# Performance work log

Hardware: AMD Instinct MI355X
Metric: run time of the kernel (lower is better)

The kernel has to match this reference:

```python
import jax, jax.numpy as jnp
import numpy as np

THRESHOLD = 0.95
SECONDARY = 0.5


def setup_inputs() -> dict:
    key = jax.random.key(0)
    quantum_states = jax.random.normal(key, (8, 2048, 64), dtype=jnp.float32)
    return {"quantum_states": quantum_states}


def reference(quantum_states):
    # quantum_states: (B, N, D)
    B, N, D = quantum_states.shape
    # pairwise fidelity: (states @ states^T)^2 -> (B, N, N)
    dots = jnp.einsum("bnd,bmd->bnm", quantum_states, quantum_states)
    fid = dots * dots
    # edge weights: 1.0 if fid >= threshold, else SECONDARY if fid >= secondary, else 0
    w = jnp.where(fid >= THRESHOLD, jnp.float32(1.0),
                  jnp.where(fid >= SECONDARY, jnp.float32(SECONDARY), jnp.float32(0.0)))
    # zero out diagonal (only i < j pairs form edges)
    eye = jnp.eye(N, dtype=bool)
    w = jnp.where(eye[None, :, :], jnp.float32(0.0), w)
    # Laplacian L = D - W
    deg = jnp.sum(w, axis=-1)  # (B, N)
    lap = -w
    idx = jnp.arange(N)
    lap = lap.at[:, idx, idx].set(deg)
    return lap
```

## Files before the change

kernel.cpp:

```cpp
#include <hip/hip_runtime.h>

typedef __attribute__((ext_vector_type(8))) __bf16 bf16x8;
typedef __attribute__((ext_vector_type(4))) __bf16 bf16x4;
typedef __attribute__((ext_vector_type(4))) float f32x4;

#define LDST 72

__global__ __launch_bounds__(256) void lap_strip_kernel(
    const float* __restrict__ X, float* __restrict__ out, int N)
{
    const int b      = blockIdx.y;
    const int strip0 = blockIdx.x * 32;
    const int tid  = threadIdx.x;
    const int lane = tid & 63;
    const int w    = tid >> 6;
    const int t    = lane & 15;
    const int g    = lane >> 4;

    __shared__ __align__(16) unsigned short As[2][128 * LDST];
    __shared__ __align__(16) unsigned short Bs[32 * LDST];
    __shared__ float deg_part[4][32];

    const float* Xb   = X   + (size_t)b * N * 64;
    float*       outb = out + (size_t)b * N * N;

    {
        const float4* src = reinterpret_cast<const float4*>(Xb + (size_t)strip0 * 64);
#pragma unroll
        for (int it = 0; it < 2; ++it) {
            int idx = tid + it * 256;
            int r = idx >> 4, q = idx & 15;
            float4 v = src[idx];
            bf16x4 h = {(__bf16)v.x, (__bf16)v.y, (__bf16)v.z, (__bf16)v.w};
            *reinterpret_cast<bf16x4*>(&Bs[r * LDST + q * 4]) = h;
        }
    }

    float4 pre[8];
    {
        const float4* src = reinterpret_cast<const float4*>(Xb);
#pragma unroll
        for (int it = 0; it < 8; ++it) pre[it] = src[tid + it * 256];
#pragma unroll
        for (int it = 0; it < 8; ++it) {
            int idx = tid + it * 256;
            int r = idx >> 4, q = idx & 15;
            float4 v = pre[it];
            bf16x4 h = {(__bf16)v.x, (__bf16)v.y, (__bf16)v.z, (__bf16)v.w};
            *reinterpret_cast<bf16x4*>(&As[0][r * LDST + q * 4]) = h;
        }
    }
    __syncthreads();

    bf16x8 bfrag[2][2];
#pragma unroll
    for (int ks = 0; ks < 2; ++ks)
#pragma unroll
        for (int fj = 0; fj < 2; ++fj)
            bfrag[ks][fj] = *reinterpret_cast<const bf16x8*>(
                &Bs[(16 * fj + t) * LDST + ks * 32 + g * 8]);

    float rs[2] = {0.f, 0.f};
    int cur = 0;
    const int nct = N >> 7;
    const int diag_ct = strip0 >> 7;

    for (int ct = 0; ct < nct; ++ct) {
        if (ct + 1 < nct) {
            const float4* src = reinterpret_cast<const float4*>(Xb + (size_t)(ct + 1) * 128 * 64);
#pragma unroll
            for (int it = 0; it < 8; ++it) pre[it] = src[tid + it * 256];
        }

        f32x4 acc[2][2] = {};
#pragma unroll
        for (int ks = 0; ks < 2; ++ks) {
            const int koff = ks * 32 + g * 8;
            bf16x8 a[2];
#pragma unroll
            for (int fi = 0; fi < 2; ++fi)
                a[fi] = *reinterpret_cast<const bf16x8*>(
                    &As[cur][(32 * w + 16 * fi + t) * LDST + koff]);
#pragma unroll
            for (int fi = 0; fi < 2; ++fi)
#pragma unroll
                for (int fj = 0; fj < 2; ++fj)
                    acc[fi][fj] = __builtin_amdgcn_mfma_f32_16x16x32_bf16(
                        a[fi], bfrag[ks][fj], acc[fi][fj], 0, 0, 0);
        }

        const bool has_diag = (ct == diag_ct);
#pragma unroll
        for (int fj = 0; fj < 2; ++fj) {
            const int orow = strip0 + 16 * fj + t;
#pragma unroll
            for (int fi = 0; fi < 2; ++fi) {
                const int ocol0 = ct * 128 + 32 * w + 16 * fi + 4 * g;
                float wv[4];
#pragma unroll
                for (int r = 0; r < 4; ++r) {
                    const float d = acc[fi][fj][r];
                    float wt = (fabsf(d) >= 0.97467943f) ? 1.0f
                             : ((fabsf(d) >= 0.70710678f) ? 0.5f : 0.0f);
                    if (has_diag && (ocol0 + r == orow)) wt = 0.0f;
                    rs[fj] += wt;
                    wv[r] = -wt;
                }
                f32x4 st = {wv[0], wv[1], wv[2], wv[3]};
                f32x4* dst = reinterpret_cast<f32x4*>(&outb[(size_t)orow * N + ocol0]);
                if (has_diag) *dst = st;
                else __builtin_nontemporal_store(st, dst);
            }
        }

        if (ct + 1 < nct) {
#pragma unroll
            for (int it = 0; it < 8; ++it) {
                int idx = tid + it * 256;
                int r = idx >> 4, q = idx & 15;
                float4 v = pre[it];
                bf16x4 h = {(__bf16)v.x, (__bf16)v.y, (__bf16)v.z, (__bf16)v.w};
                *reinterpret_cast<bf16x4*>(&As[cur ^ 1][r * LDST + q * 4]) = h;
            }
        }
        __syncthreads();
        cur ^= 1;
    }

    rs[0] += __shfl_xor(rs[0], 16, 64); rs[0] += __shfl_xor(rs[0], 32, 64);
    rs[1] += __shfl_xor(rs[1], 16, 64); rs[1] += __shfl_xor(rs[1], 32, 64);
    if (g == 0) { deg_part[w][t] = rs[0]; deg_part[w][16 + t] = rs[1]; }
    __syncthreads();
    if (tid < 32) {
        float d = deg_part[0][tid] + deg_part[1][tid] + deg_part[2][tid] + deg_part[3][tid];
        const int rr = strip0 + tid;
        outb[(size_t)rr * N + rr] = d;
    }
}

extern "C" void kernel_launch(void* const* d_in, const int* in_sizes, int n_in,
                              void* d_out, int out_size, void* d_ws, size_t ws_size,
                              hipStream_t stream) {
    const float* X = (const float*)d_in[0];
    float* out = (float*)d_out;

    const int B = 8;
    const int D = 64;
    const int N = in_sizes[0] / (B * D);

    dim3 grid(N / 32, B);
    lap_strip_kernel<<<grid, dim3(256), 0, stream>>>(X, out, N);
}
```

Before: 34.96 us.

## Use 512-thread blocks with one 16-column fragment per wave and custom barriers

Doubles the block to 8 waves, and each wave now computes a single 16-column fragment per 128-column tile instead of two, so per-thread register use and work per wave both shrink. Batch and strip are interleaved in a flat 1D grid so that neighbouring blocks come from different batches. __syncthreads is replaced with an LDS-only waitcnt plus s_barrier inside the loop, which keeps outstanding global stores and prefetch loads from stalling the barrier. In exchange there are more waves to synchronize per tile, and less MFMA work per wave to hide latency.

```diff
diff --git a/kernel.cpp b/kernel.cpp
--- a/kernel.cpp
+++ b/kernel.cpp
@@ -6,11 +6,23 @@
 
 #define LDST 72
 
-__global__ __launch_bounds__(256) void lap_strip_kernel(
+__device__ __forceinline__ void lds_barrier() {
+    asm volatile("s_waitcnt lgkmcnt(0)" ::: "memory");
+    __builtin_amdgcn_s_barrier();
+    __builtin_amdgcn_sched_barrier(0);
+}
+__device__ __forceinline__ void full_barrier() {
+    asm volatile("s_waitcnt vmcnt(0) lgkmcnt(0)" ::: "memory");
+    __builtin_amdgcn_s_barrier();
+    __builtin_amdgcn_sched_barrier(0);
+}
+
+__global__ __launch_bounds__(512) void lap_strip_kernel(
     const float* __restrict__ X, float* __restrict__ out, int N)
 {
-    const int b      = blockIdx.y;
-    const int strip0 = blockIdx.x * 32;
+    const int flat   = blockIdx.x;
+    const int b      = flat & 7;
+    const int strip0 = (flat >> 3) * 32;
     const int tid  = threadIdx.x;
     const int lane = tid & 63;
     const int w    = tid >> 6;
@@ -19,38 +31,34 @@
 
     __shared__ __align__(16) unsigned short As[2][128 * LDST];
     __shared__ __align__(16) unsigned short Bs[32 * LDST];
-    __shared__ float deg_part[4][32];
+    __shared__ float deg_part[8][32];
 
     const float* Xb   = X   + (size_t)b * N * 64;
     float*       outb = out + (size_t)b * N * N;
 
     {
         const float4* src = reinterpret_cast<const float4*>(Xb + (size_t)strip0 * 64);
-#pragma unroll
-        for (int it = 0; it < 2; ++it) {
-            int idx = tid + it * 256;
-            int r = idx >> 4, q = idx & 15;
-            float4 v = src[idx];
-            bf16x4 h = {(__bf16)v.x, (__bf16)v.y, (__bf16)v.z, (__bf16)v.w};
-            *reinterpret_cast<bf16x4*>(&Bs[r * LDST + q * 4]) = h;
-        }
+        int r = tid >> 4, q = tid & 15;
+        float4 v = src[tid];
+        bf16x4 h = {(__bf16)v.x, (__bf16)v.y, (__bf16)v.z, (__bf16)v.w};
+        *reinterpret_cast<bf16x4*>(&Bs[r * LDST + q * 4]) = h;
     }
 
-    float4 pre[8];
+    float4 pre[4];
     {
         const float4* src = reinterpret_cast<const float4*>(Xb);
 #pragma unroll
-        for (int it = 0; it < 8; ++it) pre[it] = src[tid + it * 256];
+        for (int it = 0; it < 4; ++it) pre[it] = src[tid + it * 512];
 #pragma unroll
-        for (int it = 0; it < 8; ++it) {
-            int idx = tid + it * 256;
+        for (int it = 0; it < 4; ++it) {
+            int idx = tid + it * 512;
             int r = idx >> 4, q = idx & 15;
             float4 v = pre[it];
             bf16x4 h = {(__bf16)v.x, (__bf16)v.y, (__bf16)v.z, (__bf16)v.w};
             *reinterpret_cast<bf16x4*>(&As[0][r * LDST + q * 4]) = h;
         }
     }
-    __syncthreads();
+    lds_barrier();
 
     bf16x8 bfrag[2][2];
 #pragma unroll
@@ -69,70 +77,64 @@
         if (ct + 1 < nct) {
             const float4* src = reinterpret_cast<const float4*>(Xb + (size_t)(ct + 1) * 128 * 64);
 #pragma unroll
-            for (int it = 0; it < 8; ++it) pre[it] = src[tid + it * 256];
+            for (int it = 0; it < 4; ++it) pre[it] = src[tid + it * 512];
         }
 
-        f32x4 acc[2][2] = {};
+        f32x4 acc[2] = {};
 #pragma unroll
         for (int ks = 0; ks < 2; ++ks) {
             const int koff = ks * 32 + g * 8;
-            bf16x8 a[2];
+            bf16x8 a = *reinterpret_cast<const bf16x8*>(
+                &As[cur][(16 * w + t) * LDST + koff]);
 #pragma unroll
-            for (int fi = 0; fi < 2; ++fi)
-                a[fi] = *reinterpret_cast<const bf16x8*>(
-                    &As[cur][(32 * w + 16 * fi + t) * LDST + koff]);
-#pragma unroll
-            for (int fi = 0; fi < 2; ++fi)
-#pragma unroll
-                for (int fj = 0; fj < 2; ++fj)
-                    acc[fi][fj] = __builtin_amdgcn_mfma_f32_16x16x32_bf16(
-                        a[fi], bfrag[ks][fj], acc[fi][fj], 0, 0, 0);
+            for (int fj = 0; fj < 2; ++fj)
+                acc[fj] = __builtin_amdgcn_mfma_f32_16x16x32_bf16(
+                    a, bfrag[ks][fj], acc[fj], 0, 0, 0);
         }
 
         const bool has_diag = (ct == diag_ct);
 #pragma unroll
         for (int fj = 0; fj < 2; ++fj) {
-            const int orow = strip0 + 16 * fj + t;
+            const int orow  = strip0 + 16 * fj + t;
+            const int ocol0 = ct * 128 + 16 * w + 4 * g;
+            float wv[4];
 #pragma unroll
-            for (int fi = 0; fi < 2; ++fi) {
-                const int ocol0 = ct * 128 + 32 * w + 16 * fi + 4 * g;
-                float wv[4];
-#pragma unroll
-                for (int r = 0; r < 4; ++r) {
-                    const float d = acc[fi][fj][r];
-                    float wt = (fabsf(d) >= 0.97467943f) ? 1.0f
-                             : ((fabsf(d) >= 0.70710678f) ? 0.5f : 0.0f);
-                    if (has_diag && (ocol0 + r == orow)) wt = 0.0f;
-                    rs[fj] += wt;
-                    wv[r] = -wt;
-                }
-                f32x4 st = {wv[0], wv[1], wv[2], wv[3]};
-                f32x4* dst = reinterpret_cast<f32x4*>(&outb[(size_t)orow * N + ocol0]);
-                if (has_diag) *dst = st;
-                else __builtin_nontemporal_store(st, dst);
+            for (int r = 0; r < 4; ++r) {
+                const float d = acc[fj][r];
+                float wt = (fabsf(d) >= 0.97467943f) ? 1.0f
+                         : ((fabsf(d) >= 0.70710678f) ? 0.5f : 0.0f);
+                if (has_diag && (ocol0 + r == orow)) wt = 0.0f;
+                rs[fj] += wt;
+                wv[r] = -wt;
             }
+            f32x4 st = {wv[0], wv[1], wv[2], wv[3]};
+            f32x4* dst = reinterpret_cast<f32x4*>(&outb[(size_t)orow * N + ocol0]);
+            if (has_diag) *dst = st;
+            else __builtin_nontemporal_store(st, dst);
         }
 
         if (ct + 1 < nct) {
 #pragma unroll
-            for (int it = 0; it < 8; ++it) {
-                int idx = tid + it * 256;
+            for (int it = 0; it < 4; ++it) {
+                int idx = tid + it * 512;
                 int r = idx >> 4, q = idx & 15;
                 float4 v = pre[it];
                 bf16x4 h = {(__bf16)v.x, (__bf16)v.y, (__bf16)v.z, (__bf16)v.w};
                 *reinterpret_cast<bf16x4*>(&As[cur ^ 1][r * LDST + q * 4]) = h;
             }
         }
-        __syncthreads();
+        lds_barrier();
         cur ^= 1;
     }
 
     rs[0] += __shfl_xor(rs[0], 16, 64); rs[0] += __shfl_xor(rs[0], 32, 64);
     rs[1] += __shfl_xor(rs[1], 16, 64); rs[1] += __shfl_xor(rs[1], 32, 64);
     if (g == 0) { deg_part[w][t] = rs[0]; deg_part[w][16 + t] = rs[1]; }
-    __syncthreads();
+    full_barrier();
     if (tid < 32) {
-        float d = deg_part[0][tid] + deg_part[1][tid] + deg_part[2][tid] + deg_part[3][tid];
+        float d = 0.f;
+#pragma unroll
+        for (int ww = 0; ww < 8; ++ww) d += deg_part[ww][tid];
         const int rr = strip0 + tid;
         outb[(size_t)rr * N + rr] = d;
     }
@@ -148,6 +150,6 @@
     const int D = 64;
     const int N = in_sizes[0] / (B * D);
 
-    dim3 grid(N / 32, B);
-    lap_strip_kernel<<<grid, dim3(256), 0, stream>>>(X, out, N);
+    dim3 grid((N / 32) * B);
+    lap_strip_kernel<<<grid, dim3(512), 0, stream>>>(X, out, N);
 }
```

Result: no change. 34.32 us (-1.8%).
